# Kernel tuning notes

Measured on AMD Instinct MI355X. Metric: run time of the kernel, lower is better.

The kernel has to match this reference:

```python
import jax, jax.numpy as jnp
import numpy as np

N_NODES = 100000
N_EDGES = 640000
IN_CH, HID_CH, OUT_CH = 256, 128, 64


def setup_inputs() -> dict:
    key = jax.random.key(0)
    ks = jax.random.split(key, 6)
    x = jax.random.normal(ks[0], (N_NODES, IN_CH), dtype=jnp.float32)
    edge_index = jax.random.randint(ks[1], (2, N_EDGES), 0, N_NODES, dtype=jnp.int32)
    # Glorot-style init for GCNConv weights
    W1 = jax.random.normal(ks[2], (IN_CH, HID_CH), dtype=jnp.float32) * (1.0 / np.sqrt(IN_CH))
    W_mu = jax.random.normal(ks[3], (HID_CH, OUT_CH), dtype=jnp.float32) * (1.0 / np.sqrt(HID_CH))
    W_logvar = jax.random.normal(ks[4], (HID_CH, OUT_CH), dtype=jnp.float32) * (1.0 / np.sqrt(HID_CH))
    return {
        "x": x,
        "edge_index": edge_index,
        "W1": W1,
        "b1": jnp.zeros((HID_CH,), jnp.float32),
        "W_mu": W_mu,
        "b_mu": jnp.zeros((OUT_CH,), jnp.float32),
        "W_logvar": W_logvar,
        "b_logvar": jnp.zeros((OUT_CH,), jnp.float32),
    }


def reference(x, edge_index, W1, b1, W_mu, b_mu, W_logvar, b_logvar):
    N = x.shape[0]
    # PyG GCNConv default: add self-loops, symmetric normalization D^-1/2 A_hat D^-1/2
    loops = jnp.arange(N, dtype=edge_index.dtype)
    src = jnp.concatenate([edge_index[0], loops])  # [E+N]
    dst = jnp.concatenate([edge_index[1], loops])  # [E+N]
    deg = jax.ops.segment_sum(jnp.ones_like(src, dtype=x.dtype), dst, num_segments=N)
    dinv = jax.lax.rsqrt(deg)  # deg >= 1 due to self-loops
    norm = dinv[src] * dinv[dst]  # [E+N]

    def gcn_conv(h, W, b):
        h = h @ W                                   # [N, d_out]
        msg = h[src] * norm[:, None]                # gather + scale  [E+N, d_out]
        out = jax.ops.segment_sum(msg, dst, num_segments=N)  # scatter-add
        return out + b

    h = jax.nn.relu(gcn_conv(x, W1, b1))
    mu = gcn_conv(h, W_mu, b_mu)
    logvar = gcn_conv(h, W_logvar, b_logvar)
    return (mu, logvar)
```

## Files before the change

kernel.cpp:

```cpp
#include <hip/hip_runtime.h>
#include <hip/hip_bf16.h>

#define N_NODES 100000
#define E_EDGES 640000

typedef __attribute__((ext_vector_type(8))) short short8;
typedef __attribute__((ext_vector_type(4))) float float4v;

__device__ __forceinline__ float bf2f(unsigned int u16) {
    union { unsigned int i; float f; } c; c.i = u16 << 16; return c.f;
}
__device__ __forceinline__ unsigned short f2bf(float f) {
    union { float f; unsigned int i; } c; c.f = f;
    unsigned int x = c.i;
    unsigned int r = (x + 0x7fffu + ((x >> 16) & 1u)) >> 16;
    return (unsigned short)r;
}

#define ASYNC16(g, l)                                                          \
    __builtin_amdgcn_global_load_lds(                                          \
        (const __attribute__((address_space(1))) void*)(g),                    \
        (__attribute__((address_space(3))) void*)(l), 16, 0, 0)

#define WS_HIST    0
#define WS_CURSOR  524288
#define WS_OFFS    1048576
#define WS_DINV    1572864
#define WS_BSUMS   2097152
#define WS_EIDX    2621440
#define WS_WP1     7864320
#define WS_WP2     7929856
#define WS_H0      7962624
#define WS_H       33562624

#define NB_E 2500
__global__ __launch_bounds__(256) void k_hist_pack(const int* __restrict__ dst, int* __restrict__ hist,
                                                   const float* __restrict__ W1,
                                                   const float* __restrict__ Wmu,
                                                   const float* __restrict__ Wlv,
                                                   unsigned short* __restrict__ Wp1,
                                                   unsigned short* __restrict__ Wp2) {
    int b = blockIdx.x;
    if (b < NB_E) {
        int e = b * 256 + threadIdx.x;
        if (e < E_EDGES) atomicAdd(&hist[dst[e]], 1);
    } else {
        int i = (b - NB_E) * 256 + threadIdx.x;
        if (i < 256 * 128) {
            int k = i >> 7, n = i & 127;
            Wp1[n * 256 + k] = f2bf(W1[i]);
        }
        if (i < 128 * 128) {
            int k = i >> 7, n = i & 127;
            float w = (n < 64) ? Wmu[k * 64 + n] : Wlv[k * 64 + (n - 64)];
            Wp2[n * 128 + k] = f2bf(w);
        }
    }
}

__global__ __launch_bounds__(256) void k_scan1(const int* __restrict__ hist,
                                               int* __restrict__ offs,
                                               int* __restrict__ bsums,
                                               float* __restrict__ dinv) {
    __shared__ int sd[256];
    int t = threadIdx.x;
    int base = blockIdx.x * 1024 + t * 4;
    int v[4];
#pragma unroll
    for (int j = 0; j < 4; ++j) v[j] = (base + j < N_NODES) ? hist[base + j] : 0;
#pragma unroll
    for (int j = 0; j < 4; ++j)
        if (base + j < N_NODES) dinv[base + j] = rsqrtf((float)(v[j] + 1));
    int s = v[0] + v[1] + v[2] + v[3];
    sd[t] = s;
    __syncthreads();
    for (int d = 1; d < 256; d <<= 1) {
        int x = (t >= d) ? sd[t - d] : 0;
        __syncthreads();
        sd[t] += x;
        __syncthreads();
    }
    int excl = sd[t] - s;
    if (t == 255) bsums[blockIdx.x] = sd[255];
    int run = excl;
#pragma unroll
    for (int j = 0; j < 4; ++j) {
        if (base + j < N_NODES) offs[base + j] = run;
        run += v[j];
    }
}

__global__ __launch_bounds__(128) void k_scan2(int* __restrict__ bsums, int nb) {
    __shared__ int sd[128];
    int t = threadIdx.x;
    int v = (t < nb) ? bsums[t] : 0;
    sd[t] = v;
    __syncthreads();
    for (int d = 1; d < 128; d <<= 1) {
        int x = (t >= d) ? sd[t - d] : 0;
        __syncthreads();
        sd[t] += x;
        __syncthreads();
    }
    if (t < nb) bsums[t] = sd[t] - v;
}

__global__ __launch_bounds__(256) void k_fill(const int* __restrict__ src, const int* __restrict__ dst,
                                              const int* __restrict__ offs, const int* __restrict__ bsums,
                                              int* __restrict__ cursor,
                                              const float* __restrict__ dinv,
                                              int2* __restrict__ eidx) {
    int e = blockIdx.x * 256 + threadIdx.x;
    if (e < E_EDGES) {
        int s = src[e], d = dst[e];
        int p = offs[d] + bsums[d >> 10] + atomicAdd(&cursor[d], 1);
        int2 v;
        v.x = s;
        v.y = __float_as_int(dinv[s] * dinv[d]);
        eidx[p] = v;
    }
}

__global__ __launch_bounds__(256, 6) void k_mgemm1(const float* __restrict__ A,
                                                   const unsigned short* __restrict__ Bpack,
                                                   unsigned short* __restrict__ out) {
    __shared__ float As[64 * 32];
    __shared__ unsigned short Bs[128 * 40];
    int tid = threadIdx.x;
    int row0 = blockIdx.x * 64;
    int wave = tid >> 6, lane = tid & 63;
    int c = lane & 15, q = lane >> 4;
    int wrow = (wave >> 1) * 32, wcol = (wave & 1) * 64;

    float4v acc[2][4];
#pragma unroll
    for (int i = 0; i < 2; ++i)
#pragma unroll
        for (int j = 0; j < 4; ++j) acc[i][j] = (float4v){0.f, 0.f, 0.f, 0.f};

    int srow = tid >> 1;
    int shalf = (tid & 1) * 16;

    for (int k0 = 0; k0 < 256; k0 += 32) {
        const unsigned short* bsrc = Bpack + (size_t)srow * 256 + k0 + shalf;
        short8 b0 = *(const short8*)(bsrc);
        short8 b1 = *(const short8*)(bsrc + 8);
#pragma unroll
        for (int t = 0; t < 2; ++t) {
            int grp = t * 4 + wave;
            int S = grp * 64 + lane;
            int row = S >> 3, j = S & 7;
            int kq = j ^ (row & 7);
            const float* g = A + (size_t)(row0 + row) * 256 + k0 + kq * 4;
            float* ldst = As + grp * 256;
            if (row0 + row < N_NODES) ASYNC16(g, ldst);
        }
        *(short8*)(&Bs[srow * 40 + shalf])     = b0;
        *(short8*)(&Bs[srow * 40 + shalf + 8]) = b1;
        __syncthreads();

        short8 af[2], bfr[4];
#pragma unroll
        for (int mt = 0; mt < 2; ++mt) {
            int r = wrow + mt * 16 + c;
            int j0 = (q * 2) ^ (r & 7);
            float4v fa = *(const float4v*)(&As[r * 32 + j0 * 4]);
            float4v fb = *(const float4v*)(&As[r * 32 + (j0 ^ 1) * 4]);
            short8 s;
#pragma unroll
            for (int jj = 0; jj < 4; ++jj) s[jj]     = (short)f2bf(fa[jj]);
#pragma unroll
            for (int jj = 0; jj < 4; ++jj) s[4 + jj] = (short)f2bf(fb[jj]);
            af[mt] = s;
        }
#pragma unroll
        for (int nt = 0; nt < 4; ++nt)
            bfr[nt] = *(const short8*)(&Bs[(wcol + nt * 16 + c) * 40 + q * 8]);
#pragma unroll
        for (int mt = 0; mt < 2; ++mt)
#pragma unroll
            for (int nt = 0; nt < 4; ++nt)
                acc[mt][nt] = __builtin_amdgcn_mfma_f32_16x16x32_bf16(af[mt], bfr[nt], acc[mt][nt], 0, 0, 0);
        __syncthreads();
    }

#pragma unroll
    for (int mt = 0; mt < 2; ++mt) {
#pragma unroll
        for (int i = 0; i < 4; ++i) {
            int row = row0 + wrow + mt * 16 + q * 4 + i;
            if (row >= N_NODES) continue;
#pragma unroll
            for (int nt = 0; nt < 4; ++nt) {
                int cc = wcol + nt * 16 + c;
                out[(size_t)row * 128 + cc] = f2bf(acc[mt][nt][i]);
            }
        }
    }
}

__global__ __launch_bounds__(256, 6) void k_mgemm2(const unsigned short* __restrict__ A,
                                                   const unsigned short* __restrict__ Bpack,
                                                   const float* __restrict__ bias0,
                                                   const float* __restrict__ bias1,
                                                   float* __restrict__ out) {
    constexpr int LDT = 40;
    __shared__ unsigned short As[64 * LDT];
    __shared__ unsigned short Bs[128 * LDT];
    int tid = threadIdx.x;
    int row0 = blockIdx.x * 64;
    int wave = tid >> 6, lane = tid & 63;
    int c = lane & 15, q = lane >> 4;
    int wrow = (wave >> 1) * 32, wcol = (wave & 1) * 64;

    float4v acc[2][4];
#pragma unroll
    for (int i = 0; i < 2; ++i)
#pragma unroll
        for (int j = 0; j < 4; ++j) acc[i][j] = (float4v){0.f, 0.f, 0.f, 0.f};

    int srow = tid >> 1, shalf = (tid & 1) * 16;
    int arow = tid >> 2, aoff = (tid & 3) * 8;
    const short8 zed = {0, 0, 0, 0, 0, 0, 0, 0};

    for (int k0 = 0; k0 < 128; k0 += 32) {
        const unsigned short* bsrc = Bpack + (size_t)srow * 128 + k0 + shalf;
        short8 b0 = *(const short8*)(bsrc);
        short8 b1 = *(const short8*)(bsrc + 8);
        int grow = row0 + arow;
        short8 a0 = zed;
        if (grow < N_NODES)
            a0 = *(const short8*)(A + (size_t)grow * 128 + k0 + aoff);
        *(short8*)(&Bs[srow * LDT + shalf])     = b0;
        *(short8*)(&Bs[srow * LDT + shalf + 8]) = b1;
        *(short8*)(&As[arow * LDT + aoff])      = a0;
        __syncthreads();

        short8 af[2], bfr[4];
#pragma unroll
        for (int mt = 0; mt < 2; ++mt)
            af[mt] = *(const short8*)(&As[(wrow + mt * 16 + c) * LDT + q * 8]);
#pragma unroll
        for (int nt = 0; nt < 4; ++nt)
            bfr[nt] = *(const short8*)(&Bs[(wcol + nt * 16 + c) * LDT + q * 8]);
#pragma unroll
        for (int mt = 0; mt < 2; ++mt)
#pragma unroll
            for (int nt = 0; nt < 4; ++nt)
                acc[mt][nt] = __builtin_amdgcn_mfma_f32_16x16x32_bf16(af[mt], bfr[nt], acc[mt][nt], 0, 0, 0);
        __syncthreads();
    }

#pragma unroll
    for (int mt = 0; mt < 2; ++mt) {
#pragma unroll
        for (int i = 0; i < 4; ++i) {
            int row = row0 + wrow + mt * 16 + q * 4 + i;
            if (row >= N_NODES) continue;
#pragma unroll
            for (int nt = 0; nt < 4; ++nt) {
                int cc = wcol + nt * 16 + c;
                float v = acc[mt][nt][i];
                if (cc < 64) out[(size_t)row * 64 + cc] = v + bias0[cc];
                else out[(size_t)N_NODES * 64 + (size_t)row * 64 + (cc - 64)] = v + bias1[cc - 64];
            }
        }
    }
}

template <int BIAS_RELU>
__global__ __launch_bounds__(256) void k_agg(const unsigned int* __restrict__ in,
                                             unsigned int* __restrict__ out,
                                             const float* __restrict__ dinv,
                                             const int2* __restrict__ eidx,
                                             const int* __restrict__ offs,
                                             const int* __restrict__ bsums,
                                             const int* __restrict__ cnt,
                                             const float* __restrict__ bias) {
    int wid = (blockIdx.x * 256 + threadIdx.x) >> 6;
    if (wid >= N_NODES) return;
    int l = threadIdx.x & 63;
    float di = dinv[wid];
    unsigned int u = in[(size_t)wid * 64 + l];
    float sc = di * di;
    float ax = sc * bf2f(u & 0xffffu);
    float ay = sc * bf2f(u >> 16);
    if (BIAS_RELU) { ax += bias[2 * l]; ay += bias[2 * l + 1]; }
    int start = offs[wid] + bsums[wid >> 10];
    int n = cnt[wid];

    for (int base = 0; base < n; base += 64) {
        int m = min(n - base, 64);
        int sreg = 0; float wreg = 0.f;
        if (l < m) {
            int2 ev = eidx[start + base + l];
            sreg = ev.x;
            wreg = __int_as_float(ev.y);
        }
        int e = 0;
        for (; e + 4 <= m; e += 4) {
            int s0 = __shfl(sreg, e),     s1 = __shfl(sreg, e + 1);
            int s2 = __shfl(sreg, e + 2), s3 = __shfl(sreg, e + 3);
            float w0 = __shfl(wreg, e),     w1 = __shfl(wreg, e + 1);
            float w2 = __shfl(wreg, e + 2), w3 = __shfl(wreg, e + 3);
            unsigned int u0 = in[(size_t)s0 * 64 + l];
            unsigned int u1 = in[(size_t)s1 * 64 + l];
            unsigned int u2 = in[(size_t)s2 * 64 + l];
            unsigned int u3 = in[(size_t)s3 * 64 + l];
            ax += w0 * bf2f(u0 & 0xffffu); ay += w0 * bf2f(u0 >> 16);
            ax += w1 * bf2f(u1 & 0xffffu); ay += w1 * bf2f(u1 >> 16);
            ax += w2 * bf2f(u2 & 0xffffu); ay += w2 * bf2f(u2 >> 16);
            ax += w3 * bf2f(u3 & 0xffffu); ay += w3 * bf2f(u3 >> 16);
        }
        for (; e < m; ++e) {
            int s0 = __shfl(sreg, e);
            float w0 = __shfl(wreg, e);
            unsigned int u0 = in[(size_t)s0 * 64 + l];
            ax += w0 * bf2f(u0 & 0xffffu); ay += w0 * bf2f(u0 >> 16);
        }
    }
    if (BIAS_RELU) { ax = fmaxf(ax, 0.f); ay = fmaxf(ay, 0.f); }
    out[(size_t)wid * 64 + l] = (unsigned int)f2bf(ax) | ((unsigned int)f2bf(ay) << 16);
}

extern "C" void kernel_launch(void* const* d_in, const int* in_sizes, int n_in,
                              void* d_out, int out_size, void* d_ws, size_t ws_size,
                              hipStream_t stream) {
    const float* x    = (const float*)d_in[0];
    const int*   ei   = (const int*)d_in[1];
    const float* W1   = (const float*)d_in[2];
    const float* b1   = (const float*)d_in[3];
    const float* Wmu  = (const float*)d_in[4];
    const float* bmu  = (const float*)d_in[5];
    const float* Wlv  = (const float*)d_in[6];
    const float* blv  = (const float*)d_in[7];
    float* outp = (float*)d_out;

    const int* src = ei;
    const int* dst = ei + E_EDGES;

    char* ws = (char*)d_ws;
    int*            hist   = (int*)(ws + WS_HIST);
    int*            cursor = (int*)(ws + WS_CURSOR);
    int*            offs   = (int*)(ws + WS_OFFS);
    float*          dinv   = (float*)(ws + WS_DINV);
    int*            bsums  = (int*)(ws + WS_BSUMS);
    int2*           eidx   = (int2*)(ws + WS_EIDX);
    unsigned short* Wp1    = (unsigned short*)(ws + WS_WP1);
    unsigned short* Wp2    = (unsigned short*)(ws + WS_WP2);
    unsigned short* h0     = (unsigned short*)(ws + WS_H0);
    unsigned short* h      = (unsigned short*)(ws + WS_H);

    const int NB_S = (N_NODES + 1023) / 1024;
    const int NB_G = (N_NODES + 63) / 64;

    hipMemsetAsync(ws + WS_HIST, 0, 1048576, stream);
    k_hist_pack<<<NB_E + 128, 256, 0, stream>>>(dst, hist, W1, Wmu, Wlv, Wp1, Wp2);
    k_scan1<<<NB_S, 256, 0, stream>>>(hist, offs, bsums, dinv);
    k_scan2<<<1, 128, 0, stream>>>(bsums, NB_S);
    k_fill<<<NB_E, 256, 0, stream>>>(src, dst, offs, bsums, cursor, dinv, eidx);

    k_mgemm1<<<NB_G, 256, 0, stream>>>(x, Wp1, h0);
    k_agg<1><<<(N_NODES * 64 + 255) / 256, 256, 0, stream>>>(
        (const unsigned int*)h0, (unsigned int*)h, dinv, eidx, offs, bsums, hist, b1);

    k_agg<0><<<(N_NODES * 64 + 255) / 256, 256, 0, stream>>>(
        (const unsigned int*)h, (unsigned int*)h0, dinv, eidx, offs, bsums, hist, nullptr);
    k_mgemm2<<<NB_G, 256, 0, stream>>>(h0, Wp2, bmu, blv, outp);
}
```

Measured before the change: 352.8 us.

## Load GEMM operands directly from global into MFMA fragments, dropping LDS staging

Both dense GEMM kernels stop staging A and B tiles through shared memory with barriers. Each lane now loads its MFMA fragments straight from global memory inside a fully unrolled K loop. This removes the LDS traffic, the async copies and the syncthreads, and lets the compiler hoist and overlap all loads. The cost is redundant global and L2 reads, since B and A rows are shared across waves, and possibly higher register pressure.

Measured after the change: 374.4 us. 6.1% more time.

```diff
diff --git a/kernel.cpp b/kernel.cpp
--- a/kernel.cpp
+++ b/kernel.cpp
@@ -16,11 +16,6 @@
     unsigned int r = (x + 0x7fffu + ((x >> 16) & 1u)) >> 16;
     return (unsigned short)r;
 }
-
-#define ASYNC16(g, l)                                                          \
-    __builtin_amdgcn_global_load_lds(                                          \
-        (const __attribute__((address_space(1))) void*)(g),                    \
-        (__attribute__((address_space(3))) void*)(l), 16, 0, 0)
 
 #define WS_HIST    0
 #define WS_CURSOR  524288
@@ -121,11 +116,9 @@
     }
 }
 
-__global__ __launch_bounds__(256, 6) void k_mgemm1(const float* __restrict__ A,
-                                                   const unsigned short* __restrict__ Bpack,
-                                                   unsigned short* __restrict__ out) {
-    __shared__ float As[64 * 32];
-    __shared__ unsigned short Bs[128 * 40];
+__global__ __launch_bounds__(256) void k_mgemm1(const float* __restrict__ A,
+                                                const unsigned short* __restrict__ Bpack,
+                                                unsigned short* __restrict__ out) {
     int tid = threadIdx.x;
     int row0 = blockIdx.x * 64;
     int wave = tid >> 6, lane = tid & 63;
@@ -138,58 +131,55 @@
 #pragma unroll
         for (int j = 0; j < 4; ++j) acc[i][j] = (float4v){0.f, 0.f, 0.f, 0.f};
 
-    int srow = tid >> 1;
-    int shalf = (tid & 1) * 16;
-
-    for (int k0 = 0; k0 < 256; k0 += 32) {
-        const unsigned short* bsrc = Bpack + (size_t)srow * 256 + k0 + shalf;
-        short8 b0 = *(const short8*)(bsrc);
-        short8 b1 = *(const short8*)(bsrc + 8);
-#pragma unroll
-        for (int t = 0; t < 2; ++t) {
-            int grp = t * 4 + wave;
-            int S = grp * 64 + lane;
-            int row = S >> 3, j = S & 7;
-            int kq = j ^ (row & 7);
-            const float* g = A + (size_t)(row0 + row) * 256 + k0 + kq * 4;
-            float* ldst = As + grp * 256;
-            if (row0 + row < N_NODES) ASYNC16(g, ldst);
-        }
-        *(short8*)(&Bs[srow * 40 + shalf])     = b0;
-        *(short8*)(&Bs[srow * 40 + shalf + 8]) = b1;
-        __syncthreads();
-
+    bool val[2];
+    const float* aptr[2];
+#pragma unroll
+    for (int mt = 0; mt < 2; ++mt) {
+        int base = row0 + wrow + mt * 16;
+        val[mt] = (base < N_NODES);
+        int r = val[mt] ? (base + c) : 0;
+        aptr[mt] = A + (size_t)r * 256 + q * 8;
+    }
+    const unsigned short* bptr[4];
+#pragma unroll
+    for (int nt = 0; nt < 4; ++nt)
+        bptr[nt] = Bpack + (size_t)(wcol + nt * 16 + c) * 256 + q * 8;
+
+#pragma unroll
+    for (int kc = 0; kc < 8; ++kc) {
         short8 af[2], bfr[4];
 #pragma unroll
+        for (int nt = 0; nt < 4; ++nt)
+            bfr[nt] = *(const short8*)(bptr[nt] + kc * 32);
+#pragma unroll
         for (int mt = 0; mt < 2; ++mt) {
-            int r = wrow + mt * 16 + c;
-            int j0 = (q * 2) ^ (r & 7);
-            float4v fa = *(const float4v*)(&As[r * 32 + j0 * 4]);
-            float4v fb = *(const float4v*)(&As[r * 32 + (j0 ^ 1) * 4]);
+            float4v fa = (float4v){0.f, 0.f, 0.f, 0.f};
+            float4v fb = (float4v){0.f, 0.f, 0.f, 0.f};
+            if (val[mt]) {
+                fa = *(const float4v*)(aptr[mt] + kc * 32);
+                fb = *(const float4v*)(aptr[mt] + kc * 32 + 4);
+            }
             short8 s;
 #pragma unroll
-            for (int jj = 0; jj < 4; ++jj) s[jj]     = (short)f2bf(fa[jj]);
-#pragma unroll
-            for (int jj = 0; jj < 4; ++jj) s[4 + jj] = (short)f2bf(fb[jj]);
+            for (int jj = 0; jj < 4; ++jj) {
+                s[jj]     = (short)f2bf(fa[jj]);
+                s[4 + jj] = (short)f2bf(fb[jj]);
+            }
             af[mt] = s;
         }
-#pragma unroll
-        for (int nt = 0; nt < 4; ++nt)
-            bfr[nt] = *(const short8*)(&Bs[(wcol + nt * 16 + c) * 40 + q * 8]);
 #pragma unroll
         for (int mt = 0; mt < 2; ++mt)
 #pragma unroll
             for (int nt = 0; nt < 4; ++nt)
                 acc[mt][nt] = __builtin_amdgcn_mfma_f32_16x16x32_bf16(af[mt], bfr[nt], acc[mt][nt], 0, 0, 0);
-        __syncthreads();
     }
 
 #pragma unroll
     for (int mt = 0; mt < 2; ++mt) {
+        if (!val[mt]) continue;
 #pragma unroll
         for (int i = 0; i < 4; ++i) {
             int row = row0 + wrow + mt * 16 + q * 4 + i;
-            if (row >= N_NODES) continue;
 #pragma unroll
             for (int nt = 0; nt < 4; ++nt) {
                 int cc = wcol + nt * 16 + c;
@@ -199,14 +189,11 @@
     }
 }
 
-__global__ __launch_bounds__(256, 6) void k_mgemm2(const unsigned short* __restrict__ A,
-                                                   const unsigned short* __restrict__ Bpack,
-                                                   const float* __restrict__ bias0,
-                                                   const float* __restrict__ bias1,
-                                                   float* __restrict__ out) {
-    constexpr int LDT = 40;
-    __shared__ unsigned short As[64 * LDT];
-    __shared__ unsigned short Bs[128 * LDT];
+__global__ __launch_bounds__(256) void k_mgemm2(const unsigned short* __restrict__ A,
+                                                const unsigned short* __restrict__ Bpack,
+                                                const float* __restrict__ bias0,
+                                                const float* __restrict__ bias1,
+                                                float* __restrict__ out) {
     int tid = threadIdx.x;
     int row0 = blockIdx.x * 64;
     int wave = tid >> 6, lane = tid & 63;
@@ -219,44 +206,45 @@
 #pragma unroll
         for (int j = 0; j < 4; ++j) acc[i][j] = (float4v){0.f, 0.f, 0.f, 0.f};
 
-    int srow = tid >> 1, shalf = (tid & 1) * 16;
-    int arow = tid >> 2, aoff = (tid & 3) * 8;
-    const short8 zed = {0, 0, 0, 0, 0, 0, 0, 0};
-
-    for (int k0 = 0; k0 < 128; k0 += 32) {
-        const unsigned short* bsrc = Bpack + (size_t)srow * 128 + k0 + shalf;
-        short8 b0 = *(const short8*)(bsrc);
-        short8 b1 = *(const short8*)(bsrc + 8);
-        int grow = row0 + arow;
-        short8 a0 = zed;
-        if (grow < N_NODES)
-            a0 = *(const short8*)(A + (size_t)grow * 128 + k0 + aoff);
-        *(short8*)(&Bs[srow * LDT + shalf])     = b0;
-        *(short8*)(&Bs[srow * LDT + shalf + 8]) = b1;
-        *(short8*)(&As[arow * LDT + aoff])      = a0;
-        __syncthreads();
-
+    bool val[2];
+    const unsigned short* aptr[2];
+#pragma unroll
+    for (int mt = 0; mt < 2; ++mt) {
+        int base = row0 + wrow + mt * 16;
+        val[mt] = (base < N_NODES);
+        int r = val[mt] ? (base + c) : 0;
+        aptr[mt] = A + (size_t)r * 128 + q * 8;
+    }
+    const unsigned short* bptr[4];
+#pragma unroll
+    for (int nt = 0; nt < 4; ++nt)
+        bptr[nt] = Bpack + (size_t)(wcol + nt * 16 + c) * 128 + q * 8;
+
+#pragma unroll
+    for (int kc = 0; kc < 4; ++kc) {
         short8 af[2], bfr[4];
 #pragma unroll
-        for (int mt = 0; mt < 2; ++mt)
-            af[mt] = *(const short8*)(&As[(wrow + mt * 16 + c) * LDT + q * 8]);
-#pragma unroll
         for (int nt = 0; nt < 4; ++nt)
-            bfr[nt] = *(const short8*)(&Bs[(wcol + nt * 16 + c) * LDT + q * 8]);
+            bfr[nt] = *(const short8*)(bptr[nt] + kc * 32);
+#pragma unroll
+        for (int mt = 0; mt < 2; ++mt) {
+            short8 a = {0, 0, 0, 0, 0, 0, 0, 0};
+            if (val[mt]) a = *(const short8*)(aptr[mt] + kc * 32);
+            af[mt] = a;
+        }
 #pragma unroll
         for (int mt = 0; mt < 2; ++mt)
 #pragma unroll
             for (int nt = 0; nt < 4; ++nt)
                 acc[mt][nt] = __builtin_amdgcn_mfma_f32_16x16x32_bf16(af[mt], bfr[nt], acc[mt][nt], 0, 0, 0);
-        __syncthreads();
     }
 
 #pragma unroll
     for (int mt = 0; mt < 2; ++mt) {
+        if (!val[mt]) continue;
 #pragma unroll
         for (int i = 0; i < 4; ++i) {
             int row = row0 + wrow + mt * 16 + q * 4 + i;
-            if (row >= N_NODES) continue;
 #pragma unroll
             for (int nt = 0; nt < 4; ++nt) {
                 int cc = wcol + nt * 16 + c;
```
